# Kernel optimization log

Measured on AMD Instinct MI355X. Metric: run time of the kernel, lower is better.

## Reference

```python
import jax, jax.numpy as jnp
import numpy as np

R = 32
BN_EPS = 1e-5


def _bn(x, g, b):
    # eval-mode BatchNorm with running_mean=0, running_var=1
    shp = (1, -1) + (1,) * (x.ndim - 2)
    scale = g / np.float32(np.sqrt(1.0 + BN_EPS))
    return x * scale.reshape(shp) + b.reshape(shp)


def _conv3d(x, w, b):
    y = jax.lax.conv_general_dilated(x, w, (1, 1, 1), [(1, 1)] * 3,
                                     dimension_numbers=('NCDHW', 'OIDHW', 'NCDHW'))
    return y + b[None, :, None, None, None]


def _conv1d(x, w, b):  # kernel_size=1 conv -> matmul; w [O,I], x [B,I,N]
    return jnp.einsum('oi,bin->bon', w, x) + b[None, :, None]


def _voxelize(features, coords, r):
    # PVCNN Voxelization: detach coords, center, normalize, scatter-average
    coords = jax.lax.stop_gradient(coords)
    c = coords - coords.mean(axis=2, keepdims=True)            # [B,3,N]
    nrm = jnp.linalg.norm(c, axis=1, keepdims=True)            # [B,1,N]
    c = c / (nrm.max(axis=2, keepdims=True) * 2.0) + 0.5
    c = jnp.clip(c * r, 0.0, r - 1.0)                          # float voxel coords
    vox = jnp.round(c).astype(jnp.int32)
    B, C, N = features.shape
    idx = vox[:, 0] * r * r + vox[:, 1] * r + vox[:, 2]        # [B,N]
    flat = (idx + (jnp.arange(B, dtype=jnp.int32) * (r ** 3))[:, None]).reshape(-1)
    feats = features.transpose(0, 2, 1).reshape(B * N, C)
    sums = jax.ops.segment_sum(feats, flat, num_segments=B * r ** 3)
    cnt = jax.ops.segment_sum(jnp.ones((B * N,), features.dtype), flat, num_segments=B * r ** 3)
    grid = sums / jnp.maximum(cnt, 1.0)[:, None]
    grid = grid.reshape(B, r, r, r, C).transpose(0, 4, 1, 2, 3)  # [B,C,r,r,r]
    return grid, c


def _devoxelize(grid, c, r):
    # trilinear interpolation gather at float coords c in [0, r-1]
    B, C = grid.shape[:2]
    lo = jnp.clip(jnp.floor(c).astype(jnp.int32), 0, r - 1)
    hi = jnp.minimum(lo + 1, r - 1)
    f = c - lo.astype(c.dtype)
    gridf = grid.reshape(B, C, r * r * r)
    gather = jax.vmap(lambda g, i: g[:, i])  # per-batch [C,R3],[N] -> [C,N]
    out = jnp.zeros((B, C, c.shape[2]), grid.dtype)
    for ix, wx in ((lo[:, 0], 1.0 - f[:, 0]), (hi[:, 0], f[:, 0])):
        for iy, wy in ((lo[:, 1], 1.0 - f[:, 1]), (hi[:, 1], f[:, 1])):
            for iz, wz in ((lo[:, 2], 1.0 - f[:, 2]), (hi[:, 2], f[:, 2])):
                idx = ix * r * r + iy * r + iz
                out = out + gather(gridf, idx) * (wx * wy * wz)[:, None, :]
    return out


def setup_inputs() -> dict:
    key = jax.random.key(0)
    ks = jax.random.split(key, 24)
    n = lambda k, s, sc=0.05: (jax.random.normal(k, s, dtype=jnp.float32) * sc)
    inp = {
        'features': jax.random.normal(ks[0], (4, 64, 65536), dtype=jnp.float32),
        'coords': jax.random.normal(ks[1], (4, 3, 65536), dtype=jnp.float32),
        'vconv_w': n(ks[2], (64, 64, 3, 3, 3)),
        'vconv_b': n(ks[3], (64,)),
        'vbn_g': 1.0 + n(ks[4], (64,)),
        'vbn_b': n(ks[5], (64,)),
        'res_w': n(ks[6], (2, 2, 64, 64, 3, 3, 3)),
        'res_b': n(ks[7], (2, 2, 64)),
        'res_bn_g': 1.0 + n(ks[8], (2, 2, 64)),
        'res_bn_b': n(ks[9], (2, 2, 64)),
        'pf_w': n(ks[10], (64, 64)),
        'pf_b': n(ks[11], (64,)),
        'pf_bn_g': 1.0 + n(ks[12], (64,)),
        'pf_bn_b': n(ks[13], (64,)),
        'attn_wa': n(ks[14], (16, 64)),
        'attn_ba': n(ks[15], (16,)),
        'attn_wb': n(ks[16], (16, 64)),
        'attn_bb': n(ks[17], (16,)),
        'attn_wc': n(ks[18], (1, 32)),
        'attn_bc': n(ks[19], (1,)),
    }
    return inp


def reference(features, coords, vconv_w, vconv_b, vbn_g, vbn_b,
              res_w, res_b, res_bn_g, res_bn_b,
              pf_w, pf_b, pf_bn_g, pf_bn_b,
              attn_wa, attn_ba, attn_wb, attn_bb, attn_wc, attn_bc):
    grid, nc = _voxelize(features, coords, R)
    # BasicConvolutionBlock
    x = jax.nn.relu(_bn(_conv3d(grid, vconv_w, vconv_b), vbn_g, vbn_b))
    # two ResidualBlocks (inc==outc, stride 1 -> identity downsample)
    for i in range(2):
        y = jax.nn.relu(_bn(_conv3d(x, res_w[i, 0], res_b[i, 0]), res_bn_g[i, 0], res_bn_b[i, 0]))
        y = _bn(_conv3d(y, res_w[i, 1], res_b[i, 1]), res_bn_g[i, 1], res_bn_b[i, 1])
        x = jax.nn.relu(y + x)
    vfeat = _devoxelize(x, nc, R)                               # [B,64,N]
    # SharedMLP: Conv1d(k=1) + BN1d + ReLU
    pfeat = jax.nn.relu(_bn(_conv1d(features, pf_w, pf_b), pf_bn_g, pf_bn_b))
    # Attn fusion (channel dim 64 -> atten_64 branch)
    xa = _conv1d(vfeat, attn_wa, attn_ba)
    xb = _conv1d(pfeat, attn_wb, attn_bb)
    q = _conv1d(jnp.concatenate([xa, xb], axis=1), attn_wc, attn_bc)
    attention = 1.0 + jax.nn.sigmoid(q)
    fused = vfeat * attention + pfeat
    return fused
```

## Files before the change

### kernel.cpp

```cpp
#include <hip/hip_runtime.h>
#include <math.h>

#define NPT 65536
#define NB 4
#define R3 32768

typedef __attribute__((ext_vector_type(8))) short short8;
typedef __attribute__((ext_vector_type(16))) float f32x16;

#define OFF_WB16 0
#define OFF_BEFF 276480
#define OFF_PWB  276800
#define OFF_PB   280896
#define OFF_WAE  280960
#define OFF_WBE  281024
#define OFF_Q0   281088
#define OFF_MEAN 281104
#define OFF_MAXN 281116
#define OFF_PART 281120
#define OFF_AUX  281248
#define OFF_CB3  281504
#define OFF_CUR  1067936
#define OFF_ORD  1199008
#define OFF_GA   1330080
#define OFF_G0   9718688
#define OFF_G1   13912992

__device__ __forceinline__ unsigned short f2b(float f) {
    union { float f; unsigned int u; } v; v.f = f;
    unsigned int r = v.u + 0x7fffu + ((v.u >> 16) & 1u);
    return (unsigned short)(r >> 16);
}
__device__ __forceinline__ float b2f(unsigned short u) {
    union { unsigned int u; float f; } v; v.u = ((unsigned int)u) << 16; return v.f;
}

__global__ void k_fold_w(const float* __restrict__ vconv_w, const float* __restrict__ vbn_g,
                         const float* __restrict__ res_w, const float* __restrict__ res_bn_g,
                         unsigned short* __restrict__ wb16) {
    int idx = blockIdx.x * 256 + threadIdx.x;
    if (idx >= 5 * 27 * 4 * 2 * 64 * 8) return;
    int j = idx & 7;
    int l = (idx >> 3) & 63;
    int nh = (idx >> 9) & 1;
    int ks = (idx >> 10) & 3;
    int rest = idx >> 12;
    int t = rest % 27;
    int layer = rest / 27;
    int i = ks * 16 + ((l >> 5) << 3) + j;
    int o = nh * 32 + (l & 31);
    const float invs = rsqrtf(1.00001f);
    float scale, wsrc;
    if (layer == 0) {
        scale = vbn_g[o] * invs;
        wsrc = vconv_w[(o * 64 + i) * 27 + t];
    } else {
        scale = res_bn_g[(layer - 1) * 64 + o] * invs;
        wsrc = res_w[(size_t)(layer - 1) * 110592 + (o * 64 + i) * 27 + t];
    }
    wb16[idx] = f2b(wsrc * scale);
}

__global__ void k_misc(const float* __restrict__ vconv_b, const float* __restrict__ vbn_g,
                       const float* __restrict__ vbn_b,
                       const float* __restrict__ res_b, const float* __restrict__ res_bn_g,
                       const float* __restrict__ res_bn_b,
                       const float* __restrict__ pf_w, const float* __restrict__ pf_b,
                       const float* __restrict__ pf_bn_g, const float* __restrict__ pf_bn_b,
                       const float* __restrict__ wa, const float* __restrict__ ba,
                       const float* __restrict__ wb, const float* __restrict__ bb,
                       const float* __restrict__ wc, const float* __restrict__ bc,
                       float* __restrict__ ws) {
    int idx = blockIdx.x * 256 + threadIdx.x;
    const float invs = rsqrtf(1.00001f);
    if (idx < 320) {
        int l = idx >> 6, o = idx & 63;
        float b_, g_, s_;
        if (l == 0) { b_ = vconv_b[o]; g_ = vbn_g[o]; s_ = vbn_b[o]; }
        else {
            b_ = res_b[(l - 1) * 64 + o];
            g_ = res_bn_g[(l - 1) * 64 + o];
            s_ = res_bn_b[(l - 1) * 64 + o];
        }
        ws[OFF_BEFF + idx] = b_ * g_ * invs + s_;
    } else if (idx < 4416) {
        int e = idx - 320;
        int j = e & 7;
        int lane = (e >> 3) & 63;
        int ks = (e >> 9) & 3;
        int half = e >> 11;
        int i = ks * 16 + ((lane >> 5) << 3) + j;
        int o = half * 32 + (lane & 31);
        ((unsigned short*)(ws + OFF_PWB))[e] = f2b(pf_w[o * 64 + i] * pf_bn_g[o] * invs);
    } else if (idx < 4480) {
        int o = idx - 4416;
        ws[OFF_PB + o] = pf_b[o] * pf_bn_g[o] * invs + pf_bn_b[o];
    } else if (idx < 4544) {
        int o = idx - 4480;
        float s = 0.f;
        for (int j = 0; j < 16; j++) s += wc[j] * wa[j * 64 + o];
        ws[OFF_WAE + o] = s;
    } else if (idx < 4608) {
        int o = idx - 4544;
        float s = 0.f;
        for (int j = 0; j < 16; j++) s += wc[16 + j] * wb[j * 64 + o];
        ws[OFF_WBE + o] = s;
    } else if (idx == 4608) {
        float s = bc[0];
        for (int j = 0; j < 16; j++) s += wc[j] * ba[j] + wc[16 + j] * bb[j];
        ws[OFF_Q0] = s;
    }
}

__global__ void k_zero(float4* __restrict__ p, int n4) {
    int i = blockIdx.x * 256 + threadIdx.x;
    if (i < n4) p[i] = make_float4(0.f, 0.f, 0.f, 0.f);
}

__global__ __launch_bounds__(256) void k_mean1(const float* __restrict__ coords,
                                               float* __restrict__ part) {
    __shared__ float sm[256];
    int bd = blockIdx.x >> 3, chunk = blockIdx.x & 7;
    int tid = threadIdx.x;
    const float* p = coords + (size_t)bd * NPT + chunk * 8192;
    float s = 0.f;
    for (int n = tid; n < 8192; n += 256) s += p[n];
    sm[tid] = s; __syncthreads();
    for (int st = 128; st > 0; st >>= 1) {
        if (tid < st) sm[tid] += sm[tid + st];
        __syncthreads();
    }
    if (tid == 0) part[blockIdx.x] = sm[0];
}

__global__ void k_mean2(const float* __restrict__ part, float* __restrict__ mean) {
    int t = threadIdx.x;
    if (t < 12) {
        float s = 0.f;
        for (int c = 0; c < 8; c++) s += part[t * 8 + c];
        mean[t] = s * (1.0f / NPT);
    }
}

__global__ __launch_bounds__(256) void k_maxn1(const float* __restrict__ coords,
                                               const float* __restrict__ mean,
                                               float* __restrict__ part) {
    __shared__ float sm[256];
    int b = blockIdx.x >> 3, chunk = blockIdx.x & 7;
    int tid = threadIdx.x;
    float m0 = mean[b * 3], m1 = mean[b * 3 + 1], m2 = mean[b * 3 + 2];
    const float* p0 = coords + (size_t)(b * 3) * NPT + chunk * 8192;
    float mx = 0.f;
    for (int n = tid; n < 8192; n += 256) {
        float dx = p0[n] - m0, dy = p0[NPT + n] - m1, dz = p0[2 * NPT + n] - m2;
        mx = fmaxf(mx, dx * dx + dy * dy + dz * dz);
    }
    sm[tid] = mx; __syncthreads();
    for (int st = 128; st > 0; st >>= 1) {
        if (tid < st) sm[tid] = fmaxf(sm[tid], sm[tid + st]);
        __syncthreads();
    }
    if (tid == 0) part[96 + blockIdx.x] = sm[0];
}

__global__ void k_maxn2(const float* __restrict__ part, float* __restrict__ maxn) {
    int t = threadIdx.x;
    if (t < 4) {
        float m = 0.f;
        for (int c = 0; c < 8; c++) m = fmaxf(m, part[96 + t * 8 + c]);
        maxn[t] = sqrtf(m);
    }
}

__global__ void k_prep(const float* __restrict__ coords, const float* __restrict__ mean,
                       const float* __restrict__ maxn, float* __restrict__ cb3,
                       int* __restrict__ cursor) {
    int gid = blockIdx.x * 256 + threadIdx.x;
    int b = gid >> 16, n = gid & 65535;
    float inv = 0.5f / maxn[b];
    float c0 = (coords[(size_t)(b * 3) * NPT + n]     - mean[b * 3])     * inv + 0.5f;
    float c1 = (coords[(size_t)(b * 3 + 1) * NPT + n] - mean[b * 3 + 1]) * inv + 0.5f;
    float c2 = (coords[(size_t)(b * 3 + 2) * NPT + n] - mean[b * 3 + 2]) * inv + 0.5f;
    c0 = fminf(fmaxf(c0 * 32.f, 0.f), 31.f);
    c1 = fminf(fmaxf(c1 * 32.f, 0.f), 31.f);
    c2 = fminf(fmaxf(c2 * 32.f, 0.f), 31.f);
    cb3[gid * 3]     = c0;
    cb3[gid * 3 + 1] = c1;
    cb3[gid * 3 + 2] = c2;
    int vx = b * R3 + ((int)rintf(c0) * 1024 + (int)rintf(c1) * 32 + (int)rintf(c2));
    atomicAdd(&cursor[vx], 1);
}

__global__ void k_scan1(int* __restrict__ cur, int* __restrict__ aux) {
    __shared__ int sm[256];
    int t = threadIdx.x;
    int base = blockIdx.x * 512 + t * 2;
    int c0 = cur[base], c1 = cur[base + 1];
    int s = c0 + c1;
    sm[t] = s; __syncthreads();
    for (int off = 1; off < 256; off <<= 1) {
        int v = (t >= off) ? sm[t - off] : 0;
        __syncthreads();
        sm[t] += v;
        __syncthreads();
    }
    int ex = sm[t] - s;
    cur[base] = ex;
    cur[base + 1] = ex + c0;
    if (t == 255) aux[blockIdx.x] = sm[t];
}

__global__ void k_scan2(int* __restrict__ aux) {
    __shared__ int sm[256];
    int t = threadIdx.x;
    int v0 = aux[t];
    sm[t] = v0; __syncthreads();
    for (int off = 1; off < 256; off <<= 1) {
        int v = (t >= off) ? sm[t - off] : 0;
        __syncthreads();
        sm[t] += v;
        __syncthreads();
    }
    aux[t] = sm[t] - v0;
}

__global__ void k_scan3(int* __restrict__ cur, const int* __restrict__ aux) {
    int t = threadIdx.x;
    int add = aux[blockIdx.x];
    int base = blockIdx.x * 512 + t * 2;
    cur[base] += add;
    cur[base + 1] += add;
}

__global__ __launch_bounds__(256) void k_trans(const float* __restrict__ feats,
                                               unsigned short* __restrict__ ft) {
    __shared__ float lds[64][65];
    int b = blockIdx.x >> 10;
    int n0 = (blockIdx.x & 1023) << 6;
    int tid = threadIdx.x;
    int nl = tid & 63;
    #pragma unroll
    for (int it = 0; it < 16; it++) {
        int ch = it * 4 + (tid >> 6);
        lds[nl][ch] = feats[((size_t)(b * 64 + ch) << 16) + n0 + nl];
    }
    __syncthreads();
    int nn = tid >> 2;
    int ch0 = (tid & 3) << 4;
    size_t obase = (((size_t)(b << 16) + n0 + nn) << 6) + ch0;
    short8 v0, v1;
    #pragma unroll
    for (int j = 0; j < 8; j++) v0[j] = (short)f2b(lds[nn][ch0 + j]);
    #pragma unroll
    for (int j = 0; j < 8; j++) v1[j] = (short)f2b(lds[nn][ch0 + 8 + j]);
    *(short8*)(ft + obase) = v0;
    *(short8*)(ft + obase + 8) = v1;
}

__global__ void k_place(const float* __restrict__ cb3, int* __restrict__ cursor,
                        unsigned short* __restrict__ order) {
    int gid = blockIdx.x * 256 + threadIdx.x;
    int b = gid >> 16;
    float c0 = cb3[gid * 3], c1 = cb3[gid * 3 + 1], c2 = cb3[gid * 3 + 2];
    int vx = b * R3 + ((int)rintf(c0) * 1024 + (int)rintf(c1) * 32 + (int)rintf(c2));
    int slot = atomicAdd(&cursor[vx], 1);
    order[slot] = (unsigned short)(gid & 65535);
}

__global__ __launch_bounds__(256) void k_gather(const int* __restrict__ cursor,
        const unsigned short* __restrict__ order, const unsigned short* __restrict__ ft,
        unsigned short* __restrict__ g0) {
    int tid = threadIdx.x;
    int lane = tid & 63;
    int vx = blockIdx.x * 4 + (tid >> 6);
    int e = cursor[vx];
    int s = (vx == 0) ? 0 : cursor[vx - 1];
    int cnt = e - s;
    int p = lane >> 3;
    int g = lane & 7;
    int bb = vx >> 15;
    float acc[8] = {0.f, 0.f, 0.f, 0.f, 0.f, 0.f, 0.f, 0.f};
    for (int base = s; base < e; base += 8) {
        int idx = base + p;
        if (idx < e) {
            int n = order[idx];
            const unsigned short* fp = ft + (((size_t)(bb << 16) + n) << 6) + (g << 3);
            short8 v = *(const short8*)fp;
            #pragma unroll
            for (int j = 0; j < 8; j++) acc[j] += b2f((unsigned short)v[j]);
        }
    }
    #pragma unroll
    for (int j = 0; j < 8; j++) {
        acc[j] += __shfl_xor(acc[j], 8, 64);
        acc[j] += __shfl_xor(acc[j], 16, 64);
        acc[j] += __shfl_xor(acc[j], 32, 64);
    }
    if (p == 0) {
        float inv = 1.0f / (float)max(cnt, 1);
        int col = vx >> 5, z = vx & 31;
        short8 o8;
        #pragma unroll
        for (int j = 0; j < 8; j++) o8[j] = (short)f2b(acc[j] * inv);
        *(short8*)(g0 + (size_t)col * 2048 + (g << 8) + z * 8) = o8;
    }
}

__global__ __launch_bounds__(256) void k_conv(const unsigned short* __restrict__ in,
        const unsigned short* __restrict__ w, const float* __restrict__ bias,
        const float* __restrict__ idF, float* __restrict__ outF,
        unsigned short* __restrict__ out) {
    __shared__ unsigned short sA[18 * 2048];
    int tid = threadIdx.x;
    int lane = tid & 63;
    int wid = tid >> 6;
    int cp = wid & 1;
    int nh = wid >> 1;
    int tile = blockIdx.x;
    int b = blockIdx.y;
    int x = tile >> 3;
    int y0 = (tile & 7) << 2;
    for (int s = 0; s < 18; s++) {
        int gx = x + s / 6 - 1;
        int gy = y0 + s % 6 - 1;
        float4 v = make_float4(0.f, 0.f, 0.f, 0.f);
        if ((unsigned)gx < 32u && (unsigned)gy < 32u) {
            const float4* src = (const float4*)(in + (((size_t)b * 1024 + gx * 32 + gy) << 11));
            v = src[tid];
        }
        ((float4*)(sA + s * 2048))[tid] = v;
    }
    __syncthreads();
    f32x16 accA = {}, accB = {};
    const short8 zero8 = {0, 0, 0, 0, 0, 0, 0, 0};
    int half = lane >> 5;
    #pragma unroll 1
    for (int t = 0; t < 27; t++) {
        int dxi = t / 9, dyi = (t / 3) % 3, dz = t % 3 - 1;
        int s0 = dxi * 6 + dyi + cp * 2;
        int zz = (lane & 31) + dz;
        bool zv = (unsigned)zz < 32u;
        int zc = zv ? zz : 0;
        const unsigned short* ac = sA + s0 * 2048 + (half << 8) + zc * 8;
        const unsigned short* wp = w + t * 4096 + nh * 512 + lane * 8;
        #pragma unroll
        for (int ks = 0; ks < 4; ks++) {
            short8 bf = *(const short8*)(wp + ks * 1024);
            short8 a0 = *(const short8*)(ac + ks * 512);
            short8 a1 = *(const short8*)(ac + 2048 + ks * 512);
            if (!zv) { a0 = zero8; a1 = zero8; }
            accA = __builtin_amdgcn_mfma_f32_32x32x16_bf16(a0, bf, accA, 0, 0, 0);
            accB = __builtin_amdgcn_mfma_f32_32x32x16_bf16(a1, bf, accB, 0, 0, 0);
        }
    }
    int o = nh * 32 + (lane & 31);
    float bb = bias[o];
    #pragma unroll
    for (int cc = 0; cc < 2; cc++) {
        int outcol = b * 1024 + x * 32 + (y0 + cp * 2 + cc);
        size_t obase = ((size_t)outcol << 11) + (size_t)((o >> 3) << 8) + (o & 7);
        const f32x16& acc = cc ? accB : accA;
        #pragma unroll
        for (int r = 0; r < 16; r++) {
            int z = (r & 3) + ((r >> 2) << 3) + ((lane >> 5) << 2);
            size_t oe = obase + (size_t)z * 8;
            float v = acc[r] + bb;
            if (idF) v += idF[oe];
            v = fmaxf(v, 0.f);
            out[oe] = f2b(v);
            if (outF) outF[oe] = v;
        }
    }
}

__global__ __launch_bounds__(256) void k_pfeat(const float* __restrict__ feats,
        const float* __restrict__ pb, const unsigned short* __restrict__ pwb,
        unsigned short* __restrict__ pf) {
    int tid = threadIdx.x;
    int lane = tid & 63;
    int wv = tid >> 6;
    int tile = blockIdx.x * 4 + wv;
    int b = tile >> 11;
    int n0 = (tile & 2047) << 5;
    int m = lane & 31, kg = lane >> 5;
    const float* fb = feats + ((size_t)b << 22) + n0 + m;
    f32x16 acc0 = {}, acc1 = {};
    #pragma unroll
    for (int ks = 0; ks < 4; ks++) {
        short8 af;
        #pragma unroll
        for (int j = 0; j < 8; j++)
            af[j] = (short)f2b(fb[(size_t)(ks * 16 + kg * 8 + j) << 16]);
        short8 b0 = *(const short8*)(pwb + ((size_t)(ks * 64 + lane) << 3));
        short8 b1 = *(const short8*)(pwb + ((size_t)((4 + ks) * 64 + lane) << 3));
        acc0 = __builtin_amdgcn_mfma_f32_32x32x16_bf16(af, b0, acc0, 0, 0, 0);
        acc1 = __builtin_amdgcn_mfma_f32_32x32x16_bf16(af, b1, acc1, 0, 0, 0);
    }
    int och = lane & 31;
    float bias0 = pb[och], bias1 = pb[32 + och];
    #pragma unroll
    for (int r = 0; r < 16; r++) {
        int p = (r & 3) + ((r >> 2) << 3) + ((lane >> 5) << 2);
        size_t base = ((size_t)(b << 16) + n0 + p) << 6;
        pf[base + och]      = f2b(fmaxf(acc0[r] + bias0, 0.f));
        pf[base + 32 + och] = f2b(fmaxf(acc1[r] + bias1, 0.f));
    }
}

__global__ __launch_bounds__(256) void k_final(const float* __restrict__ cb3,
        const unsigned short* __restrict__ gb, const unsigned short* __restrict__ pfeat,
        const float* __restrict__ ws, float* __restrict__ out) {
    __shared__ float sq[256];
    int tid = threadIdx.x;
    int l = tid & 63;
    int g = tid >> 6;
    int o0 = g << 4;
    int b = blockIdx.y;
    int n = (blockIdx.x << 6) + l;
    int gid = (b << 16) + n;
    float c0 = cb3[gid * 3], c1 = cb3[gid * 3 + 1], c2 = cb3[gid * 3 + 2];
    int lx = (int)floorf(c0), ly = (int)floorf(c1), lz = (int)floorf(c2);
    int hx = min(lx + 1, 31), hy = min(ly + 1, 31), hz = min(lz + 1, 31);
    float fx = c0 - (float)lx, fy = c1 - (float)ly, fz = c2 - (float)lz;
    int xs[2] = {lx, hx}; float wxx[2] = {1.f - fx, fx};
    int ys[2] = {ly, hy}; float wyy[2] = {1.f - fy, fy};
    int zs[2] = {lz, hz}; float wzz[2] = {1.f - fz, fz};
    float vf[16];
    #pragma unroll
    for (int j = 0; j < 16; j++) vf[j] = 0.f;
    #pragma unroll
    for (int ii = 0; ii < 2; ii++)
    #pragma unroll
    for (int jj = 0; jj < 2; jj++)
    #pragma unroll
    for (int kk = 0; kk < 2; kk++) {
        float wgt = wxx[ii] * wyy[jj] * wzz[kk];
        const unsigned short* gp = gb + (((size_t)b * 1024 + xs[ii] * 32 + ys[jj]) << 11)
                                      + ((size_t)g << 9) + zs[kk] * 8;
        short8 v0 = *(const short8*)(gp);
        short8 v1 = *(const short8*)(gp + 256);
        #pragma unroll
        for (int j = 0; j < 8; j++) {
            vf[j]     += wgt * b2f((unsigned short)v0[j]);
            vf[8 + j] += wgt * b2f((unsigned short)v1[j]);
        }
    }
    float pf[16];
    const unsigned short* pp = pfeat + ((size_t)gid << 6) + o0;
    short8 p0 = *(const short8*)pp;
    short8 p1 = *(const short8*)(pp + 8);
    #pragma unroll
    for (int j = 0; j < 8; j++) {
        pf[j]     = b2f((unsigned short)p0[j]);
        pf[8 + j] = b2f((unsigned short)p1[j]);
    }
    const float* wae = ws + OFF_WAE + o0;
    const float* wbe = ws + OFF_WBE + o0;
    float part = 0.f;
    #pragma unroll
    for (int j = 0; j < 16; j++) part += wae[j] * vf[j] + wbe[j] * pf[j];
    sq[tid] = part;
    __syncthreads();
    float q = sq[l] + sq[l + 64] + sq[l + 128] + sq[l + 192] + ws[OFF_Q0];
    float attn = 1.0f + 1.0f / (1.0f + expf(-q));
    float* op = out + (size_t)(b * 64 + o0) * NPT + n;
    #pragma unroll
    for (int j = 0; j < 16; j++) op[(size_t)j * NPT] = vf[j] * attn + pf[j];
}

extern "C" void kernel_launch(void* const* d_in, const int* in_sizes, int n_in,
                              void* d_out, int out_size, void* d_ws, size_t ws_size,
                              hipStream_t stream) {
    const float* features = (const float*)d_in[0];
    const float* coords   = (const float*)d_in[1];
    const float* vconv_w  = (const float*)d_in[2];
    const float* vconv_b  = (const float*)d_in[3];
    const float* vbn_g    = (const float*)d_in[4];
    const float* vbn_b    = (const float*)d_in[5];
    const float* res_w    = (const float*)d_in[6];
    const float* res_b    = (const float*)d_in[7];
    const float* res_bn_g = (const float*)d_in[8];
    const float* res_bn_b = (const float*)d_in[9];
    const float* pf_w     = (const float*)d_in[10];
    const float* pf_b     = (const float*)d_in[11];
    const float* pf_bn_g  = (const float*)d_in[12];
    const float* pf_bn_b  = (const float*)d_in[13];
    const float* attn_wa  = (const float*)d_in[14];
    const float* attn_ba  = (const float*)d_in[15];
    const float* attn_wb  = (const float*)d_in[16];
    const float* attn_bb  = (const float*)d_in[17];
    const float* attn_wc  = (const float*)d_in[18];
    const float* attn_bc  = (const float*)d_in[19];
    float* ws  = (float*)d_ws;
    float* out = (float*)d_out;

    unsigned short* WB  = (unsigned short*)(ws + OFF_WB16);
    unsigned short* PWB = (unsigned short*)(ws + OFF_PWB);
    int*            CUR = (int*)(ws + OFF_CUR);
    int*            AUX = (int*)(ws + OFF_AUX);
    unsigned short* ORD = (unsigned short*)(ws + OFF_ORD);
    unsigned short* FT  = (unsigned short*)(ws + OFF_GA);
    unsigned short* PF  = (unsigned short*)(ws + OFF_GA);
    float* GA = ws + OFF_GA;
    unsigned short* G0 = (unsigned short*)(ws + OFF_G0);
    unsigned short* G1 = (unsigned short*)(ws + OFF_G1);
    const float* Bv = ws + OFF_BEFF;

    k_fold_w<<<2160, 256, 0, stream>>>(vconv_w, vbn_g, res_w, res_bn_g, WB);
    k_misc<<<19, 256, 0, stream>>>(vconv_b, vbn_g, vbn_b, res_b, res_bn_g, res_bn_b,
                                   pf_w, pf_b, pf_bn_g, pf_bn_b,
                                   attn_wa, attn_ba, attn_wb, attn_bb, attn_wc, attn_bc, ws);
    k_zero<<<128, 256, 0, stream>>>((float4*)CUR, 32768);
    k_mean1<<<96, 256, 0, stream>>>(coords, ws + OFF_PART);
    k_mean2<<<1, 64, 0, stream>>>(ws + OFF_PART, ws + OFF_MEAN);
    k_maxn1<<<32, 256, 0, stream>>>(coords, ws + OFF_MEAN, ws + OFF_PART);
    k_maxn2<<<1, 64, 0, stream>>>(ws + OFF_PART, ws + OFF_MAXN);
    k_prep<<<1024, 256, 0, stream>>>(coords, ws + OFF_MEAN, ws + OFF_MAXN,
                                     ws + OFF_CB3, CUR);
    k_scan1<<<256, 256, 0, stream>>>(CUR, AUX);
    k_scan2<<<1, 256, 0, stream>>>(AUX);
    k_scan3<<<256, 256, 0, stream>>>(CUR, AUX);
    k_trans<<<4096, 256, 0, stream>>>(features, FT);
    k_place<<<1024, 256, 0, stream>>>(ws + OFF_CB3, CUR, ORD);
    k_gather<<<32768, 256, 0, stream>>>(CUR, ORD, FT, G0);

    dim3 cg(256, 4);
    k_conv<<<cg, 256, 0, stream>>>(G0, WB + 0 * 110592, Bv + 0,   nullptr, GA,      G1);
    k_conv<<<cg, 256, 0, stream>>>(G1, WB + 1 * 110592, Bv + 64,  nullptr, nullptr, G0);
    k_conv<<<cg, 256, 0, stream>>>(G0, WB + 2 * 110592, Bv + 128, GA,      GA,      G1);
    k_conv<<<cg, 256, 0, stream>>>(G1, WB + 3 * 110592, Bv + 192, nullptr, nullptr, G0);
    k_conv<<<cg, 256, 0, stream>>>(G0, WB + 4 * 110592, Bv + 256, GA,      nullptr, G1);

    k_pfeat<<<2048, 256, 0, stream>>>(features, ws + OFF_PB, PWB, PF);

    dim3 fg(1024, 4);
    k_final<<<fg, 256, 0, stream>>>(ws + OFF_CB3, G1, PF, ws, out);
}
```

Before: 580.5 us.

## Load conv halo via direct global-to-LDS and split final kernel channels finer

```diff
diff --git a/kernel.cpp b/kernel.cpp
--- a/kernel.cpp
+++ b/kernel.cpp
@@ -320,15 +320,20 @@
     int b = blockIdx.y;
     int x = tile >> 3;
     int y0 = (tile & 7) << 2;
+    #pragma unroll 1
     for (int s = 0; s < 18; s++) {
         int gx = x + s / 6 - 1;
         int gy = y0 + s % 6 - 1;
-        float4 v = make_float4(0.f, 0.f, 0.f, 0.f);
         if ((unsigned)gx < 32u && (unsigned)gy < 32u) {
-            const float4* src = (const float4*)(in + (((size_t)b * 1024 + gx * 32 + gy) << 11));
-            v = src[tid];
+            const unsigned short* gsrc = in + (((size_t)b * 1024 + gx * 32 + gy) << 11)
+                                            + ((size_t)tid << 3);
+            __builtin_amdgcn_global_load_lds(
+                (const __attribute__((address_space(1))) unsigned int*)gsrc,
+                (__attribute__((address_space(3))) unsigned int*)(sA + s * 2048 + (wid << 9)),
+                16, 0, 0);
+        } else {
+            ((float4*)(sA + s * 2048))[tid] = make_float4(0.f, 0.f, 0.f, 0.f);
         }
-        ((float4*)(sA + s * 2048))[tid] = v;
     }
     __syncthreads();
     f32x16 accA = {}, accB = {};
@@ -412,11 +417,10 @@
         const float* __restrict__ ws, float* __restrict__ out) {
     __shared__ float sq[256];
     int tid = threadIdx.x;
-    int l = tid & 63;
-    int g = tid >> 6;
-    int o0 = g << 4;
+    int p = tid & 31;
+    int g = tid >> 5;
     int b = blockIdx.y;
-    int n = (blockIdx.x << 6) + l;
+    int n = (blockIdx.x << 5) + p;
     int gid = (b << 16) + n;
     float c0 = cb3[gid * 3], c1 = cb3[gid * 3 + 1], c2 = cb3[gid * 3 + 2];
     int lx = (int)floorf(c0), ly = (int)floorf(c1), lz = (int)floorf(c2);
@@ -425,9 +429,9 @@
     int xs[2] = {lx, hx}; float wxx[2] = {1.f - fx, fx};
     int ys[2] = {ly, hy}; float wyy[2] = {1.f - fy, fy};
     int zs[2] = {lz, hz}; float wzz[2] = {1.f - fz, fz};
-    float vf[16];
-    #pragma unroll
-    for (int j = 0; j < 16; j++) vf[j] = 0.f;
+    float vf[8];
+    #pragma unroll
+    for (int j = 0; j < 8; j++) vf[j] = 0.f;
     #pragma unroll
     for (int ii = 0; ii < 2; ii++)
     #pragma unroll
@@ -436,36 +440,30 @@
     for (int kk = 0; kk < 2; kk++) {
         float wgt = wxx[ii] * wyy[jj] * wzz[kk];
         const unsigned short* gp = gb + (((size_t)b * 1024 + xs[ii] * 32 + ys[jj]) << 11)
-                                      + ((size_t)g << 9) + zs[kk] * 8;
-        short8 v0 = *(const short8*)(gp);
-        short8 v1 = *(const short8*)(gp + 256);
+                                      + (g << 8) + zs[kk] * 8;
+        short8 v = *(const short8*)gp;
         #pragma unroll
-        for (int j = 0; j < 8; j++) {
-            vf[j]     += wgt * b2f((unsigned short)v0[j]);
-            vf[8 + j] += wgt * b2f((unsigned short)v1[j]);
-        }
-    }
-    float pf[16];
-    const unsigned short* pp = pfeat + ((size_t)gid << 6) + o0;
-    short8 p0 = *(const short8*)pp;
-    short8 p1 = *(const short8*)(pp + 8);
-    #pragma unroll
-    for (int j = 0; j < 8; j++) {
-        pf[j]     = b2f((unsigned short)p0[j]);
-        pf[8 + j] = b2f((unsigned short)p1[j]);
-    }
-    const float* wae = ws + OFF_WAE + o0;
-    const float* wbe = ws + OFF_WBE + o0;
+        for (int j = 0; j < 8; j++) vf[j] += wgt * b2f((unsigned short)v[j]);
+    }
+    float pfv[8];
+    const unsigned short* pp = pfeat + ((size_t)gid << 6) + (g << 3);
+    short8 pv = *(const short8*)pp;
+    #pragma unroll
+    for (int j = 0; j < 8; j++) pfv[j] = b2f((unsigned short)pv[j]);
+    const float* wae = ws + OFF_WAE + (g << 3);
+    const float* wbe = ws + OFF_WBE + (g << 3);
     float part = 0.f;
     #pragma unroll
-    for (int j = 0; j < 16; j++) part += wae[j] * vf[j] + wbe[j] * pf[j];
+    for (int j = 0; j < 8; j++) part += wae[j] * vf[j] + wbe[j] * pfv[j];
     sq[tid] = part;
     __syncthreads();
-    float q = sq[l] + sq[l + 64] + sq[l + 128] + sq[l + 192] + ws[OFF_Q0];
+    float q = ws[OFF_Q0];
+    #pragma unroll
+    for (int gg = 0; gg < 8; gg++) q += sq[(gg << 5) + p];
     float attn = 1.0f + 1.0f / (1.0f + expf(-q));
-    float* op = out + (size_t)(b * 64 + o0) * NPT + n;
-    #pragma unroll
-    for (int j = 0; j < 16; j++) op[(size_t)j * NPT] = vf[j] * attn + pf[j];
+    float* op = out + (((size_t)(b * 64 + (g << 3))) << 16) + n;
+    #pragma unroll
+    for (int j = 0; j < 8; j++) op[(size_t)j << 16] = vf[j] * attn + pfv[j];
 }
 
 extern "C" void kernel_launch(void* const* d_in, const int* in_sizes, int n_in,
@@ -533,6 +531,6 @@
 
     k_pfeat<<<2048, 256, 0, stream>>>(features, ws + OFF_PB, PWB, PF);
 
-    dim3 fg(1024, 4);
+    dim3 fg(2048, 4);
     k_final<<<fg, 256, 0, stream>>>(ws + OFF_CB3, G1, PF, ws, out);
 }
```

New measurement: 563.5 us. 1.03x faster.
